# Kernel tuning notes

Hardware: AMD Instinct MI355X
Metric: run time of the kernel (lower is better)

Reference implementation:

```python
import jax, jax.numpy as jnp
import numpy as np

B, N, E = 64, 20000, 1280000

def setup_inputs() -> dict:
    key = jax.random.key(0)
    ks = jax.random.split(key, 7)
    x = jax.random.normal(ks[0], (B, N), dtype=jnp.float32)
    adj_values = jax.random.uniform(ks[1], (E,), dtype=jnp.float32)
    w = jax.random.normal(ks[2], (E,), dtype=jnp.float32)
    self_w = jax.random.normal(ks[3], (N,), dtype=jnp.float32)
    b = jax.random.normal(ks[4], (N,), dtype=jnp.float32)
    src = jax.random.randint(ks[5], (E,), 0, N, dtype=jnp.int32)
    dst = jax.random.randint(ks[6], (E,), 0, N, dtype=jnp.int32)
    return {"x": x, "adj_values": adj_values, "w": w, "self_w": self_w,
            "b": b, "src": src, "dst": dst}

def reference(x, adj_values, w, self_w, b, src, dst):
    # gather per-edge source-node features: [B, E]
    edge_vals = adj_values * x[:, src] * w
    # segment-sum over destination nodes (== sparse reduce_sum over source axis)
    # segment_sum reduces over the leading axis, so transpose to [E, B]
    ngh_sum = jax.ops.segment_sum(edge_vals.T, dst, num_segments=x.shape[1]).T  # [B, N]
    # NOTE: original module uses only inputs[0] for the self-loop (faithful quirk)
    self_loop = x[0] * self_w  # [N]
    out = ngh_sum * self_loop + b
    return jax.nn.relu(out)
```

## Files before the change

### kernel.cpp

```cpp
#include <hip/hip_runtime.h>

typedef unsigned long long u64;


#define GSZ   40
#define NG    500
#define CAP   4096
#define ETILE 2560
#define NBIN  512

__device__ __forceinline__ unsigned short f32_to_bf16(float f) {
    unsigned int u = __float_as_uint(f);
    u += 0x7FFFu + ((u >> 16) & 1u);
    return (unsigned short)(u >> 16);
}

__device__ __forceinline__ int wave_incl_scan(int v, int lane) {
#pragma unroll
    for (int d = 1; d < 64; d <<= 1) {
        int u = __shfl_up(v, d, 64);
        if (lane >= d) v += u;
    }
    return v;
}

__global__ __launch_bounds__(512) void scatter_kernel(
        const float* __restrict__ x, const float* __restrict__ adj,
        const float* __restrict__ w, const int* __restrict__ src,
        const int* __restrict__ dst, unsigned short* __restrict__ xTh,
        int* __restrict__ goff, u64* __restrict__ packed, int N, int E) {
    __shared__ u64 staged[ETILE];
    __shared__ int cnt[NBIN];
    __shared__ int ofs[NBIN];
    __shared__ int wtot[8], wbase[8];
    int t = threadIdx.x;
    int lane = t & 63, wv = t >> 6;

    if (blockIdx.x >= NG) {
        int g = blockIdx.x - NG;
        int n0 = g * GSZ;
        float (*tile)[GSZ + 1] = (float (*)[GSZ + 1])staged;
        for (int lin = t; lin < 64 * (GSZ / 4); lin += 512) {
            int q = lin % (GSZ / 4), b = lin / (GSZ / 4);
            int n = n0 + q * 4;
            if (n < N) {
                float4 v = *(const float4*)&x[(long)b * N + n];
                tile[b][q * 4 + 0] = v.x; tile[b][q * 4 + 1] = v.y;
                tile[b][q * 4 + 2] = v.z; tile[b][q * 4 + 3] = v.w;
            }
        }
        __syncthreads();
        for (int lin = t; lin < 32 * GSZ; lin += 512) {
            int bb = lin & 31, nl = lin >> 5;
            int n = n0 + nl;
            if (n < N) {
                unsigned int lo = f32_to_bf16(tile[2 * bb][nl]);
                unsigned int hi = f32_to_bf16(tile[2 * bb + 1][nl]);
                __builtin_nontemporal_store(lo | (hi << 16),
                    (unsigned int*)&xTh[(long)n * 64 + 2 * bb]);
            }
        }
        return;
    }

    int g = blockIdx.x;
    cnt[t] = 0;
    __syncthreads();

    int base = g * ETILE;
    u64 pk[5]; int gk[5]; int rk[5];
#define EDGE_REC(j, av, wval, sv, dv)                                      \
    { int d_ = (dv); float c_ = (av) * (wval);                             \
      int gg_ = d_ / GSZ;                                                  \
      pk[j] = ((u64)__float_as_uint(c_) << 32)                             \
            | (u64)(((unsigned int)(sv) << 6) | (unsigned int)(d_ - gg_ * GSZ)); \
      gk[j] = gg_; rk[j] = atomicAdd(&cnt[gg_], 1); }
#pragma unroll
    for (int kk = 0; kk < 2; ++kk) {
        int e0 = base + kk * 1024 + 2 * t;
        float2 a2 = *(const float2*)&adj[e0];
        float2 w2 = *(const float2*)&w[e0];
        int2   s2 = *(const int2*)&src[e0];
        int2   d2 = *(const int2*)&dst[e0];
        EDGE_REC(2 * kk + 0, a2.x, w2.x, s2.x, d2.x);
        EDGE_REC(2 * kk + 1, a2.y, w2.y, s2.y, d2.y);
    }
    {
        int e = base + 2048 + t;
        EDGE_REC(4, adj[e], w[e], src[e], dst[e]);
    }
#undef EDGE_REC
    __syncthreads();

    int c = cnt[t];
    int incl = wave_incl_scan(c, lane);
    if (lane == 63) wtot[wv] = incl;
    __syncthreads();
    if (t == 0) {
        int run = 0;
#pragma unroll
        for (int k = 0; k < 8; ++k) { wbase[k] = run; run += wtot[k]; }
    }
    __syncthreads();
    ofs[t] = wbase[wv] + incl - c;
    __syncthreads();

#pragma unroll
    for (int k = 0; k < 5; ++k) {
        int pos = ofs[gk[k]] + rk[k];
        staged[pos] = pk[k];
    }
    __builtin_nontemporal_store(ofs[t], &goff[g * NBIN + t]);
    __syncthreads();
    long obase = (long)g * ETILE;
#pragma unroll
    for (int k = 0; k < 5; ++k)
        __builtin_nontemporal_store(staged[k * 512 + t], &packed[obase + k * 512 + t]);
}

__global__ __launch_bounds__(1024) void sortreduce_kernel(
        const u64* __restrict__ packed, const int* __restrict__ goff,
        const unsigned short* __restrict__ xTh, const float* __restrict__ x,
        const float* __restrict__ self_w, const float* __restrict__ bias,
        float* __restrict__ out, int N) {
    __shared__ u64 rec2[CAP];
    __shared__ float sacc[GSZ * 65];
    __shared__ int rstart[NG];
    __shared__ int rpos[NBIN];
    __shared__ int hist[NBIN];
    __shared__ int hoff[NBIN + 1];
    __shared__ int wtot[8], wbase[8];
    __shared__ int dlq;
    int t = threadIdx.x, g = blockIdx.x;
    int lane = t & 63, wv = t >> 6;

    if (t < NBIN) hist[t] = 0;
    if (t == 0) dlq = 0;
    int c = 0;
    if (t < NG) {
        int s0 = goff[t * NBIN + g];
        int s1 = goff[t * NBIN + g + 1];
        rstart[t] = s0;
        c = s1 - s0;
    }
    int incl = wave_incl_scan(c, lane);
    if (t < NBIN && lane == 63) wtot[wv] = incl;
    __syncthreads();
    if (t == 0) {
        int run = 0;
#pragma unroll
        for (int k = 0; k < 8; ++k) { wbase[k] = run; run += wtot[k]; }
    }
    __syncthreads();
    if (t < NBIN) rpos[t] = wbase[wv] + incl - c;
    __syncthreads();
    int m = min(rpos[NBIN - 1], CAP);

    u64 pv[4]; int rk4[4];
#pragma unroll
    for (int k = 0; k < 4; ++k) {
        int i = (k << 10) + t;
        pv[k] = 0; rk4[k] = -1;
        if (i < m) {
            int lo = 0;
#pragma unroll
            for (int s = 256; s >= 1; s >>= 1) {
                int j = lo + s;
                if (j < NG && rpos[j] <= i) lo = j;
            }
            u64 p = packed[(long)lo * ETILE + rstart[lo] + (i - rpos[lo])];
            pv[k] = p;
            unsigned int lo32 = (unsigned int)p;
            int key = (int)(lo32 & 63u) * 12 + (int)(lo32 >> 17);
            rk4[k] = atomicAdd(&hist[key], 1);
        }
    }
    __syncthreads();

    c = (t < NBIN) ? hist[t] : 0;
    incl = wave_incl_scan(c, lane);
    if (t < NBIN && lane == 63) wtot[wv] = incl;
    __syncthreads();
    if (t == 0) {
        int run = 0;
#pragma unroll
        for (int k = 0; k < 8; ++k) { wbase[k] = run; run += wtot[k]; }
        hoff[NBIN] = m;
    }
    __syncthreads();
    if (t < NBIN) hoff[t] = wbase[wv] + incl - c;
    __syncthreads();

#pragma unroll
    for (int k = 0; k < 4; ++k) {
        if (rk4[k] >= 0) {
            u64 p = pv[k];
            unsigned int lo32 = (unsigned int)p;
            int key = (int)(lo32 & 63u) * 12 + (int)(lo32 >> 17);
            rec2[hoff[key] + rk4[k]] = (p & 0xFFFFFFFF00000000ull) | (u64)(lo32 >> 6);
        }
    }
    __syncthreads();

    for (;;) {
        int dl;
        if (lane == 0) dl = atomicAdd(&dlq, 1);
        dl = __shfl(dl, 0, 64);
        if (dl >= GSZ) break;
        int r0 = hoff[dl * 12];
        int r1 = hoff[dl * 12 + 12];
        float a0 = 0.f, a1 = 0.f;
        int r = r0;
        for (; r + 8 <= r1; r += 8) {
            u64 p[8];
#pragma unroll
            for (int k = 0; k < 8; ++k) p[k] = rec2[r + k];
            float gg[8];
#pragma unroll
            for (int k = 0; k < 8; ++k) {
                int sk = (int)(unsigned int)p[k];
                float ck = __uint_as_float((unsigned int)(p[k] >> 32));
                float xv = __uint_as_float((unsigned int)xTh[sk * 64 + lane] << 16);
                gg[k] = ck * xv;
            }
            a0 += (gg[0] + gg[1]) + (gg[2] + gg[3]);
            a1 += (gg[4] + gg[5]) + (gg[6] + gg[7]);
        }
        for (; r < r1; ++r) {
            u64 p = rec2[r];
            int sk = (int)(unsigned int)p;
            float ck = __uint_as_float((unsigned int)(p >> 32));
            float xv = __uint_as_float((unsigned int)xTh[sk * 64 + lane] << 16);
            a0 += ck * xv;
        }
        sacc[dl * 65 + lane] = a0 + a1;
    }
    __syncthreads();

    int nl = lane;
    int n = g * GSZ + nl;
    bool ok = (nl < GSZ) && (n < N);
    float sl = 0.f, bi = 0.f;
    if (ok) { sl = x[n] * self_w[n]; bi = bias[n]; }
#pragma unroll
    for (int i = 0; i < 4; ++i) {
        int b = wv * 4 + i;
        if (ok) {
            float v = sacc[nl * 65 + b] * sl + bi;
            out[(long)b * N + n] = fmaxf(v, 0.f);
        }
    }
}

extern "C" void kernel_launch(void* const* d_in, const int* in_sizes, int n_in,
                              void* d_out, int out_size, void* d_ws, size_t ws_size,
                              hipStream_t stream) {
    const float* x      = (const float*)d_in[0];
    const float* adj    = (const float*)d_in[1];
    const float* w      = (const float*)d_in[2];
    const float* self_w = (const float*)d_in[3];
    const float* bias   = (const float*)d_in[4];
    const int*   src    = (const int*)d_in[5];
    const int*   dst    = (const int*)d_in[6];

    int N = in_sizes[3];
    int E = in_sizes[1];
    (void)n_in; (void)ws_size; (void)out_size;

    u64*            packed = (u64*)d_ws;
    unsigned short* xTh    = (unsigned short*)(packed + (size_t)NG * ETILE);
    int*            goff   = (int*)(xTh + (size_t)N * 64);
    float*          out    = (float*)d_out;

    hipLaunchKernelGGL(scatter_kernel, dim3(2 * NG), dim3(512), 0, stream,
                       x, adj, w, src, dst, xTh, goff, packed, N, E);
    hipLaunchKernelGGL(sortreduce_kernel, dim3(NG), dim3(1024), 0, stream,
                       packed, goff, xTh, x, self_w, bias, out, N);
}
```

Measured before the change: 110.5 us.

## Fuse scatter and sort-reduce into one persistent kernel with a grid barrier

Merges the two kernels into a single 512-block launch. Each block first does both the bf16 transpose of x and the edge bucketing for its tile, then waits at a device-wide atomic barrier before doing the per-group sort and reduce. Shared memory is reused through a union, and the second phase now runs on 512 threads instead of 1024, so each thread handles 8 records. The aim is to remove the kernel-launch gap and tail, at the cost of an extra memset launch, a spin barrier that requires all 512 blocks to be co-resident, and half the threads in the gather phase.

```diff
diff --git a/kernel.cpp b/kernel.cpp
--- a/kernel.cpp
+++ b/kernel.cpp
@@ -5,9 +5,25 @@
 
 #define GSZ   40
 #define NG    500
+#define NBLK  512
 #define CAP   4096
 #define ETILE 2560
 #define NBIN  512
+
+struct SmemA {
+    u64 staged[ETILE];
+    int cnt[NBIN];
+    int ofs[NBIN];
+};
+struct SmemB {
+    u64 rec2[CAP];
+    float sacc[GSZ * 65];
+    int rstart[NG];
+    int rpos[NBIN];
+    int hist[NBIN];
+    int hoff[NBIN + 1];
+};
+union Smem { SmemA a; SmemB b; };
 
 __device__ __forceinline__ unsigned short f32_to_bf16(float f) {
     unsigned int u = __float_as_uint(f);
@@ -24,22 +40,22 @@
     return v;
 }
 
-__global__ __launch_bounds__(512) void scatter_kernel(
+__global__ __launch_bounds__(512, 4) void fused_kernel(
         const float* __restrict__ x, const float* __restrict__ adj,
         const float* __restrict__ w, const int* __restrict__ src,
-        const int* __restrict__ dst, unsigned short* __restrict__ xTh,
-        int* __restrict__ goff, u64* __restrict__ packed, int N, int E) {
-    __shared__ u64 staged[ETILE];
-    __shared__ int cnt[NBIN];
-    __shared__ int ofs[NBIN];
+        const int* __restrict__ dst, const float* __restrict__ self_w,
+        const float* __restrict__ bias, float* __restrict__ out,
+        unsigned short* __restrict__ xTh, int* __restrict__ goff,
+        u64* __restrict__ packed, int* __restrict__ done, int N, int E) {
+    __shared__ Smem sm;
     __shared__ int wtot[8], wbase[8];
-    int t = threadIdx.x;
+    __shared__ int dlq;
+    int t = threadIdx.x, g = blockIdx.x;
     int lane = t & 63, wv = t >> 6;
 
-    if (blockIdx.x >= NG) {
-        int g = blockIdx.x - NG;
+    if (g < NG) {
         int n0 = g * GSZ;
-        float (*tile)[GSZ + 1] = (float (*)[GSZ + 1])staged;
+        float (*tile)[GSZ + 1] = (float (*)[GSZ + 1])sm.a.staged;
         for (int lin = t; lin < 64 * (GSZ / 4); lin += 512) {
             int q = lin % (GSZ / 4), b = lin / (GSZ / 4);
             int n = n0 + q * 4;
@@ -56,95 +72,86 @@
             if (n < N) {
                 unsigned int lo = f32_to_bf16(tile[2 * bb][nl]);
                 unsigned int hi = f32_to_bf16(tile[2 * bb + 1][nl]);
-                __builtin_nontemporal_store(lo | (hi << 16),
-                    (unsigned int*)&xTh[(long)n * 64 + 2 * bb]);
-            }
-        }
-        return;
-    }
-
-    int g = blockIdx.x;
-    cnt[t] = 0;
-    __syncthreads();
-
-    int base = g * ETILE;
-    u64 pk[5]; int gk[5]; int rk[5];
+                *(unsigned int*)&xTh[(long)n * 64 + 2 * bb] = lo | (hi << 16);
+            }
+        }
+        __syncthreads();
+
+        sm.a.cnt[t] = 0;
+        __syncthreads();
+        int base = g * ETILE;
+        u64 pk[5]; int gk[5]; int rk[5];
 #define EDGE_REC(j, av, wval, sv, dv)                                      \
-    { int d_ = (dv); float c_ = (av) * (wval);                             \
-      int gg_ = d_ / GSZ;                                                  \
-      pk[j] = ((u64)__float_as_uint(c_) << 32)                             \
-            | (u64)(((unsigned int)(sv) << 6) | (unsigned int)(d_ - gg_ * GSZ)); \
-      gk[j] = gg_; rk[j] = atomicAdd(&cnt[gg_], 1); }
-#pragma unroll
-    for (int kk = 0; kk < 2; ++kk) {
-        int e0 = base + kk * 1024 + 2 * t;
-        float2 a2 = *(const float2*)&adj[e0];
-        float2 w2 = *(const float2*)&w[e0];
-        int2   s2 = *(const int2*)&src[e0];
-        int2   d2 = *(const int2*)&dst[e0];
-        EDGE_REC(2 * kk + 0, a2.x, w2.x, s2.x, d2.x);
-        EDGE_REC(2 * kk + 1, a2.y, w2.y, s2.y, d2.y);
-    }
-    {
-        int e = base + 2048 + t;
-        EDGE_REC(4, adj[e], w[e], src[e], dst[e]);
-    }
+        { int d_ = (dv); float c_ = (av) * (wval);                         \
+          int gg_ = d_ / GSZ;                                              \
+          pk[j] = ((u64)__float_as_uint(c_) << 32)                         \
+                | (u64)(((unsigned int)(sv) << 6) | (unsigned int)(d_ - gg_ * GSZ)); \
+          gk[j] = gg_; rk[j] = atomicAdd(&sm.a.cnt[gg_], 1); }
+#pragma unroll
+        for (int kk = 0; kk < 2; ++kk) {
+            int e0 = base + kk * 1024 + 2 * t;
+            float2 a2 = *(const float2*)&adj[e0];
+            float2 w2 = *(const float2*)&w[e0];
+            int2   s2 = *(const int2*)&src[e0];
+            int2   d2 = *(const int2*)&dst[e0];
+            EDGE_REC(2 * kk + 0, a2.x, w2.x, s2.x, d2.x);
+            EDGE_REC(2 * kk + 1, a2.y, w2.y, s2.y, d2.y);
+        }
+        {
+            int e = base + 2048 + t;
+            EDGE_REC(4, adj[e], w[e], src[e], dst[e]);
+        }
 #undef EDGE_REC
-    __syncthreads();
-
-    int c = cnt[t];
-    int incl = wave_incl_scan(c, lane);
-    if (lane == 63) wtot[wv] = incl;
+        __syncthreads();
+
+        int c = sm.a.cnt[t];
+        int incl = wave_incl_scan(c, lane);
+        if (lane == 63) wtot[wv] = incl;
+        __syncthreads();
+        if (t == 0) {
+            int run = 0;
+#pragma unroll
+            for (int k = 0; k < 8; ++k) { wbase[k] = run; run += wtot[k]; }
+        }
+        __syncthreads();
+        sm.a.ofs[t] = wbase[wv] + incl - c;
+        __syncthreads();
+
+#pragma unroll
+        for (int k = 0; k < 5; ++k) {
+            int pos = sm.a.ofs[gk[k]] + rk[k];
+            sm.a.staged[pos] = pk[k];
+        }
+        goff[g * NBIN + t] = sm.a.ofs[t];
+        __syncthreads();
+        long obase = (long)g * ETILE;
+#pragma unroll
+        for (int k = 0; k < 5; ++k)
+            packed[obase + k * 512 + t] = sm.a.staged[k * 512 + t];
+    }
+
+    __threadfence();
     __syncthreads();
     if (t == 0) {
-        int run = 0;
-#pragma unroll
-        for (int k = 0; k < 8; ++k) { wbase[k] = run; run += wtot[k]; }
-    }
-    __syncthreads();
-    ofs[t] = wbase[wv] + incl - c;
-    __syncthreads();
-
-#pragma unroll
-    for (int k = 0; k < 5; ++k) {
-        int pos = ofs[gk[k]] + rk[k];
-        staged[pos] = pk[k];
-    }
-    __builtin_nontemporal_store(ofs[t], &goff[g * NBIN + t]);
-    __syncthreads();
-    long obase = (long)g * ETILE;
-#pragma unroll
-    for (int k = 0; k < 5; ++k)
-        __builtin_nontemporal_store(staged[k * 512 + t], &packed[obase + k * 512 + t]);
-}
-
-__global__ __launch_bounds__(1024) void sortreduce_kernel(
-        const u64* __restrict__ packed, const int* __restrict__ goff,
-        const unsigned short* __restrict__ xTh, const float* __restrict__ x,
-        const float* __restrict__ self_w, const float* __restrict__ bias,
-        float* __restrict__ out, int N) {
-    __shared__ u64 rec2[CAP];
-    __shared__ float sacc[GSZ * 65];
-    __shared__ int rstart[NG];
-    __shared__ int rpos[NBIN];
-    __shared__ int hist[NBIN];
-    __shared__ int hoff[NBIN + 1];
-    __shared__ int wtot[8], wbase[8];
-    __shared__ int dlq;
-    int t = threadIdx.x, g = blockIdx.x;
-    int lane = t & 63, wv = t >> 6;
-
-    if (t < NBIN) hist[t] = 0;
+        __hip_atomic_fetch_add(done, 1, __ATOMIC_RELEASE, __HIP_MEMORY_SCOPE_AGENT);
+        while (__hip_atomic_load(done, __ATOMIC_ACQUIRE, __HIP_MEMORY_SCOPE_AGENT) < NBLK)
+            __builtin_amdgcn_s_sleep(2);
+    }
+    __syncthreads();
+
+    if (g >= NG) return;
+
+    sm.b.hist[t] = 0;
     if (t == 0) dlq = 0;
     int c = 0;
     if (t < NG) {
         int s0 = goff[t * NBIN + g];
         int s1 = goff[t * NBIN + g + 1];
-        rstart[t] = s0;
+        sm.b.rstart[t] = s0;
         c = s1 - s0;
     }
     int incl = wave_incl_scan(c, lane);
-    if (t < NBIN && lane == 63) wtot[wv] = incl;
+    if (lane == 63) wtot[wv] = incl;
     __syncthreads();
     if (t == 0) {
         int run = 0;
@@ -152,52 +159,53 @@
         for (int k = 0; k < 8; ++k) { wbase[k] = run; run += wtot[k]; }
     }
     __syncthreads();
-    if (t < NBIN) rpos[t] = wbase[wv] + incl - c;
-    __syncthreads();
-    int m = min(rpos[NBIN - 1], CAP);
-
-    u64 pv[4]; int rk4[4];
-#pragma unroll
-    for (int k = 0; k < 4; ++k) {
-        int i = (k << 10) + t;
-        pv[k] = 0; rk4[k] = -1;
+    sm.b.rpos[t] = wbase[wv] + incl - c;
+    __syncthreads();
+    int m = min(sm.b.rpos[NBIN - 1], CAP);
+
+    u64 pv[8]; int rk8[8];
+#pragma unroll
+    for (int k = 0; k < 8; ++k) {
+        int i = (k << 9) + t;
+        pv[k] = 0; rk8[k] = -1;
         if (i < m) {
             int lo = 0;
 #pragma unroll
             for (int s = 256; s >= 1; s >>= 1) {
                 int j = lo + s;
-                if (j < NG && rpos[j] <= i) lo = j;
-            }
-            u64 p = packed[(long)lo * ETILE + rstart[lo] + (i - rpos[lo])];
+                if (j < NG && sm.b.rpos[j] <= i) lo = j;
+            }
+            u64 p = packed[(long)lo * ETILE + sm.b.rstart[lo] + (i - sm.b.rpos[lo])];
             pv[k] = p;
             unsigned int lo32 = (unsigned int)p;
             int key = (int)(lo32 & 63u) * 12 + (int)(lo32 >> 17);
-            rk4[k] = atomicAdd(&hist[key], 1);
-        }
-    }
-    __syncthreads();
-
-    c = (t < NBIN) ? hist[t] : 0;
+            rk8[k] = atomicAdd(&sm.b.hist[key], 1);
+        }
+    }
+    __syncthreads();
+
+    c = sm.b.hist[t];
     incl = wave_incl_scan(c, lane);
-    if (t < NBIN && lane == 63) wtot[wv] = incl;
+    if (lane == 63) wtot[wv] = incl;
     __syncthreads();
     if (t == 0) {
         int run = 0;
 #pragma unroll
         for (int k = 0; k < 8; ++k) { wbase[k] = run; run += wtot[k]; }
-        hoff[NBIN] = m;
-    }
-    __syncthreads();
-    if (t < NBIN) hoff[t] = wbase[wv] + incl - c;
-    __syncthreads();
-
-#pragma unroll
-    for (int k = 0; k < 4; ++k) {
-        if (rk4[k] >= 0) {
+        sm.b.hoff[NBIN] = m;
+    }
+    __syncthreads();
+    sm.b.hoff[t] = wbase[wv] + incl - c;
+    __syncthreads();
+
+#pragma unroll
+    for (int k = 0; k < 8; ++k) {
+        if (rk8[k] >= 0) {
             u64 p = pv[k];
             unsigned int lo32 = (unsigned int)p;
             int key = (int)(lo32 & 63u) * 12 + (int)(lo32 >> 17);
-            rec2[hoff[key] + rk4[k]] = (p & 0xFFFFFFFF00000000ull) | (u64)(lo32 >> 6);
+            sm.b.rec2[sm.b.hoff[key] + rk8[k]] =
+                (p & 0xFFFFFFFF00000000ull) | (u64)(lo32 >> 6);
         }
     }
     __syncthreads();
@@ -207,14 +215,14 @@
         if (lane == 0) dl = atomicAdd(&dlq, 1);
         dl = __shfl(dl, 0, 64);
         if (dl >= GSZ) break;
-        int r0 = hoff[dl * 12];
-        int r1 = hoff[dl * 12 + 12];
+        int r0 = sm.b.hoff[dl * 12];
+        int r1 = sm.b.hoff[dl * 12 + 12];
         float a0 = 0.f, a1 = 0.f;
         int r = r0;
         for (; r + 8 <= r1; r += 8) {
             u64 p[8];
 #pragma unroll
-            for (int k = 0; k < 8; ++k) p[k] = rec2[r + k];
+            for (int k = 0; k < 8; ++k) p[k] = sm.b.rec2[r + k];
             float gg[8];
 #pragma unroll
             for (int k = 0; k < 8; ++k) {
@@ -227,13 +235,13 @@
             a1 += (gg[4] + gg[5]) + (gg[6] + gg[7]);
         }
         for (; r < r1; ++r) {
-            u64 p = rec2[r];
+            u64 p = sm.b.rec2[r];
             int sk = (int)(unsigned int)p;
             float ck = __uint_as_float((unsigned int)(p >> 32));
             float xv = __uint_as_float((unsigned int)xTh[sk * 64 + lane] << 16);
             a0 += ck * xv;
         }
-        sacc[dl * 65 + lane] = a0 + a1;
+        sm.b.sacc[dl * 65 + lane] = a0 + a1;
     }
     __syncthreads();
 
@@ -243,10 +251,10 @@
     float sl = 0.f, bi = 0.f;
     if (ok) { sl = x[n] * self_w[n]; bi = bias[n]; }
 #pragma unroll
-    for (int i = 0; i < 4; ++i) {
-        int b = wv * 4 + i;
+    for (int i = 0; i < 8; ++i) {
+        int b = wv * 8 + i;
         if (ok) {
-            float v = sacc[nl * 65 + b] * sl + bi;
+            float v = sm.b.sacc[nl * 65 + b] * sl + bi;
             out[(long)b * N + n] = fmaxf(v, 0.f);
         }
     }
@@ -270,10 +278,11 @@
     u64*            packed = (u64*)d_ws;
     unsigned short* xTh    = (unsigned short*)(packed + (size_t)NG * ETILE);
     int*            goff   = (int*)(xTh + (size_t)N * 64);
+    int*            done   = goff + (size_t)NG * NBIN;
     float*          out    = (float*)d_out;
 
-    hipLaunchKernelGGL(scatter_kernel, dim3(2 * NG), dim3(512), 0, stream,
-                       x, adj, w, src, dst, xTh, goff, packed, N, E);
-    hipLaunchKernelGGL(sortreduce_kernel, dim3(NG), dim3(1024), 0, stream,
-                       packed, goff, xTh, x, self_w, bias, out, N);
-}
+    hipMemsetAsync((void*)done, 0, sizeof(int), stream);
+    hipLaunchKernelGGL(fused_kernel, dim3(NBLK), dim3(512), 0, stream,
+                       x, adj, w, src, dst, self_w, bias, out,
+                       xTh, goff, packed, done, N, E);
+}
```

Measured after the change: 240.6 us. 2.18x slower.
